# Kernel optimization log

Hardware: AMD Instinct MI355X
Metric: run time of the kernel (lower is better)

The kernel has to match this reference:

```python
import jax, jax.numpy as jnp
import numpy as np

B, L, F, H, VOCAB = 32, 700, 4, 600, 2000  # batch, n_records(max_len), feats/record, hidden, vocab


def setup_inputs() -> dict:
    key = jax.random.key(0)
    ks = jax.random.split(key, 16)
    s = 0.02
    inp = {
        'records': jax.random.randint(ks[0], (B, L, F), 0, VOCAB, dtype=jnp.int64 if jax.config.jax_enable_x64 else jnp.int32),
        'index': jax.random.randint(ks[1], (B,), 0, L, dtype=jnp.int32),
        'emb': jax.random.normal(ks[2], (VOCAB, H), jnp.float32) * s,
        'W_relu': jax.random.normal(ks[3], (4 * H, H), jnp.float32) * s,
        'b_relu': jnp.zeros((H,), jnp.float32),
        'W_lin': jax.random.normal(ks[4], (H, H), jnp.float32) * s,
        'b_lin': jnp.zeros((H,), jnp.float32),
        'W_sig': jax.random.normal(ks[5], (2 * H, H), jnp.float32) * s,
        'b_sig': jnp.zeros((H,), jnp.float32),
        'W_ih': jax.random.normal(ks[6], (H, 4 * H), jnp.float32) * s,
        'W_hh': jax.random.normal(ks[7], (H, 4 * H), jnp.float32) * s,
        'b_ih': jnp.zeros((4 * H,), jnp.float32),
        'b_hh': jnp.zeros((4 * H,), jnp.float32),
        'W_log': jax.random.normal(ks[8], (H, L), jnp.float32) * s,
        'b_log': jnp.zeros((L,), jnp.float32),
    }
    return inp


def _select_content(records, emb, W_relu, b_relu, W_lin, b_lin, W_sig, b_sig):
    # embedding + concat of the 4 record features -> [B, L, 4H]
    embedded = emb[records]                               # [B, L, 4, H]
    emb_cat = embedded.reshape(records.shape[0], records.shape[1], -1)
    emb_relu = jax.nn.relu(emb_cat @ W_relu + b_relu)      # [B, L, H]
    emb_lin = emb_relu @ W_lin + b_lin                     # [B, L, H]
    pre_attn = jnp.einsum('bld,bmd->blm', emb_lin, emb_relu)  # [B, L, L]
    pad = (records.max(axis=2) == 0)                       # [B, L]
    mask = jnp.eye(records.shape[1], dtype=bool)[None] | pad[:, :, None] | pad[:, None, :]
    pre_attn = jnp.where(mask, -jnp.inf, pre_attn)
    attention = jax.nn.softmax(pre_attn, axis=2)
    emb_att = jnp.einsum('blm,bmd->bld', attention, emb_relu)  # [B, L, H]
    gate = jax.nn.sigmoid(jnp.concatenate([emb_relu, emb_att], axis=2) @ W_sig + b_sig)
    return gate * emb_relu                                 # selected_content [B, L, H]


def reference(records, index, emb, W_relu, b_relu, W_lin, b_lin, W_sig, b_sig,
              W_ih, W_hh, b_ih, b_hh, W_log, b_log):
    sc = _select_content(records, emb, W_relu, b_relu, W_lin, b_lin, W_sig, b_sig)
    # init_hidden
    hidden = jnp.mean(sc, axis=1)                          # [B, H]
    cell = jnp.zeros_like(hidden)
    pad_mask = (records.max(axis=2) == 0)                  # [B, L]
    # forward (one pointer step)
    b_idx = jnp.arange(records.shape[0])
    mask = pad_mask.at[b_idx, index].set(True)             # scatter_(1, index, 1)
    x = sc[b_idx, index]                                   # gather -> [B, H]
    gates = x @ W_ih + hidden @ W_hh + b_ih + b_hh         # [B, 4H]
    i, f, g, o = jnp.split(gates, 4, axis=1)               # torch LSTM gate order
    cell = jax.nn.sigmoid(f) * cell + jax.nn.sigmoid(i) * jnp.tanh(g)
    hidden = jax.nn.sigmoid(o) * jnp.tanh(cell)
    logits = hidden @ W_log + b_log                        # [B, max_len]
    masked = jnp.where(mask, -jnp.inf, logits)
    attention = jax.nn.log_softmax(masked, axis=1)         # [B, max_len]
    return attention, hidden, cell
```

## Files before the change

kernel.cpp:

```cpp
#include <hip/hip_runtime.h>
#include <math.h>

typedef unsigned short u16;
typedef _Float16 half8 __attribute__((ext_vector_type(8)));
typedef float f32x4 __attribute__((ext_vector_type(4)));

#define BB 32
#define LL 700
#define HH 600
#define VV 2000
#define H4 2400

#define O_SCAT   0L
#define O_LINH   57344000L
#define O_R1     86016000L
#define O_ATTNH  112896000L
#define O_ERT    144435200L
#define O_EMBH   171468800L
#define O_W2T    174028800L
#define O_WLT    177100800L
#define O_WST    177920000L
#define O_BL     179456000L
#define O_PAD    179458560L
#define O_GATES  179624960L
#define O_WIHT   179932160L
#define O_WLOGT  186076160L
#define O_XCAT   186977280L
#define O_HID16  187059200L
#define O_GLOG   187100160L

__device__ inline u16 f2h(float x) { _Float16 h = (_Float16)x; u16 u; __builtin_memcpy(&u, &h, 2); return u; }
__device__ inline float h2f(u16 u) { _Float16 h; __builtin_memcpy(&h, &u, 2); return (float)h; }
__device__ inline float to_f(float x) { return x; }
__device__ inline float to_f(u16 x) { return h2f(x); }

__device__ __forceinline__ void gll16(const u16* g, u16* l) {
    __builtin_amdgcn_global_load_lds(
        (__attribute__((address_space(1))) void*)g,
        (__attribute__((address_space(3))) void*)l, 16, 0, 0);
}

template<int EPI>
__global__ __launch_bounds__(512, 8) void hgemm_v3(
    const u16* __restrict__ A, const u16* __restrict__ B,
    u16* __restrict__ C16, const float* __restrict__ bias,
    const u16* __restrict__ gate, int ldg,
    int M, int N, int Kp, int lda, int ldb, int ldc,
    long sAz, long sBz, long sCz)
{
    const int bz = blockIdx.z;
    A += sAz * bz;  B += sBz * bz;  C16 += sCz * bz;

    __shared__ __align__(16) u16 As[8192];
    __shared__ __align__(16) u16 Bs[8192];

    const int tid = threadIdx.x;

    const int nx = gridDim.x, ny = gridDim.y;
    const int bid = blockIdx.y * nx + blockIdx.x;
    const int fg  = ny >> 3;
    const int gsz = nx << 3;
    int m_i, n_i;
    if (bid < fg * gsz) {
        int g = bid / gsz, r = bid - g * gsz;
        m_i = (g << 3) + (r & 7);
        n_i = r >> 3;
    } else {
        m_i = bid / nx;
        n_i = bid - m_i * nx;
    }
    const int m0 = m_i << 7, n0 = n_i << 7;

    const int wave = tid >> 6, lane = tid & 63;
    const int fr = lane & 15, q = lane >> 4;
    const int srd = (q ^ ((fr >> 1) & 3)) << 3;
    const int wm = (wave >> 2) << 6;
    const int wn = (wave & 3) << 5;

    const int srow = lane >> 2;
    const int kx   = ((lane & 3) ^ ((srow >> 1) & 3)) << 3;
    int ra = m0 + (wave << 4) + srow;   if (ra > M - 1) ra = M - 1;
    int rb = n0 + (wave << 4) + srow;   if (rb > N - 1) rb = N - 1;
    const u16* gA = A + (long)ra * lda + kx;
    const u16* gB = B + (long)rb * ldb + kx;
    u16* sAw = (u16*)As + (wave << 9);
    u16* sBw = (u16*)Bs + (wave << 9);

    f32x4 acc[4][2];
    #pragma unroll
    for (int i = 0; i < 4; ++i)
        #pragma unroll
        for (int j = 0; j < 2; ++j) acc[i][j] = (f32x4)0.f;

    const int nk = Kp >> 5;

    gll16(gA, sAw);  gll16(gB, sBw);
    __syncthreads();

    for (int t = 0; t < nk; ++t) {
        const int cur = (t & 1) << 12;
        if (t + 1 < nk) {
            const int nxt = cur ^ 4096;
            const long ko = (long)(t + 1) << 5;
            gll16(gA + ko, sAw + nxt);  gll16(gB + ko, sBw + nxt);
        }
        half8 af[4], bf[2];
        #pragma unroll
        for (int i = 0; i < 4; ++i)
            af[i] = *(const half8*)&As[cur + ((wm + (i << 4) + fr) << 5) + srd];
        #pragma unroll
        for (int j = 0; j < 2; ++j)
            bf[j] = *(const half8*)&Bs[cur + ((wn + (j << 4) + fr) << 5) + srd];
        #pragma unroll
        for (int i = 0; i < 4; ++i)
            #pragma unroll
            for (int j = 0; j < 2; ++j)
                acc[i][j] = __builtin_amdgcn_mfma_f32_16x16x32_f16(af[i], bf[j], acc[i][j], 0, 0, 0);
        __syncthreads();
    }

    const int lr = (lane >> 4) << 2;
    #pragma unroll
    for (int j = 0; j < 2; ++j) {
        int n = n0 + wn + (j << 4) + fr;
        if (n >= N) continue;
        float bv = bias ? bias[n] : 0.f;
        #pragma unroll
        for (int i = 0; i < 4; ++i) {
            #pragma unroll
            for (int r = 0; r < 4; ++r) {
                int m = m0 + wm + (i << 4) + lr + r;
                if (m >= M) continue;
                long off = (long)m * ldc + n;
                float v = acc[i][j][r] + bv;
                if (EPI == 1) C16[off] = f2h(v);
                if (EPI == 2) {
                    float sg = 1.f / (1.f + expf(-v));
                    C16[off] = f2h(sg * h2f(gate[(long)m * ldg + n]));
                }
            }
        }
    }
}

__global__ __launch_bounds__(256) void sgemm_k(
    const u16* __restrict__ A, const u16* __restrict__ B, float* __restrict__ C,
    int N, int Kseg, int lda, int ldb, int ldc)
{
    const int wave = threadIdx.x >> 6, lane = threadIdx.x & 63;
    const int fr = lane & 15, q8 = (lane >> 4) << 3;
    int n = blockIdx.x * 64 + wave * 16 + fr;
    int nc = (n < N) ? n : N - 1;
    const int k0 = blockIdx.y * Kseg;
    const u16* pa0 = A + (long)fr * lda + q8;
    const u16* pa1 = A + (long)(fr + 16) * lda + q8;
    const u16* pb  = B + (long)nc * ldb + q8;
    f32x4 acc0 = (f32x4)0.f, acc1 = (f32x4)0.f;
    #pragma unroll 2
    for (int k = k0; k < k0 + Kseg; k += 32) {
        half8 a0 = *(const half8*)(pa0 + k);
        half8 a1 = *(const half8*)(pa1 + k);
        half8 bv = *(const half8*)(pb + k);
        acc0 = __builtin_amdgcn_mfma_f32_16x16x32_f16(a0, bv, acc0, 0, 0, 0);
        acc1 = __builtin_amdgcn_mfma_f32_16x16x32_f16(a1, bv, acc1, 0, 0, 0);
    }
    if (n >= N) return;
    const int mr = (lane >> 4) << 2;
    #pragma unroll
    for (int r = 0; r < 4; ++r) {
        atomicAdd(&C[(long)(mr + r) * ldc + n], acc0[r]);
        atomicAdd(&C[(long)(mr + r + 16) * ldc + n], acc1[r]);
    }
}

__global__ __launch_bounds__(256) void prep_k(
    const float* __restrict__ emb, const float* __restrict__ W_relu,
    const float* __restrict__ W_lin, const float* __restrict__ W_sig,
    const float* __restrict__ W_ih, const float* __restrict__ W_hh,
    const float* __restrict__ W_log, const float* __restrict__ b_lin,
    const float* __restrict__ b_ih, const float* __restrict__ b_hh,
    const float* __restrict__ b_log,
    u16* __restrict__ embh, u16* __restrict__ w2t, u16* __restrict__ wlt,
    u16* __restrict__ wst, u16* __restrict__ wiht, u16* __restrict__ wlogt,
    float* __restrict__ bl640, float* __restrict__ gates, float* __restrict__ glog)
{
    __shared__ float t[32][33];
    const int z = blockIdx.z, bx = blockIdx.x, by = blockIdx.y;
    const int tid = threadIdx.x;

    if (z == 10) {
        int r = by * 32 + (tid >> 5), c = bx * 32 + (tid & 31);
        #pragma unroll
        for (int dy = 0; dy < 32; dy += 8) {
            int rr = r + dy;
            if (rr < VV && c < 640)
                embh[(long)rr * 640 + c] = (c < 600) ? f2h(emb[(long)rr * 600 + c]) : 0;
        }
        return;
    }
    if (z == 11) {
        long idx = ((long)bx * 75 + by) * 256 + tid;
        if (idx < 640) {
            bl640[idx] = (idx < 600) ? b_lin[idx] : 0.f;
        } else if (idx < 640 + (long)BB * H4) {
            long i = idx - 640;
            int n = (int)(i % H4);
            gates[i] = b_ih[n] + b_hh[n];
        } else if (idx < 640 + (long)BB * H4 + (long)BB * 704) {
            long i = idx - 640 - (long)BB * H4;
            int l = (int)(i % 704);
            glog[i] = (l < 700) ? b_log[l] : 0.f;
        }
        return;
    }

    const float* s; u16* d;
    int R, C, lds_, ldo, Rpad, Cpad;
    if (z < 4)      { s = W_relu + 360000L * z; d = w2t + 384000L * z;
                      R = 600; C = 600; lds_ = 600; ldo = 640;  Rpad = 640; Cpad = 600; }
    else if (z == 4){ s = W_lin;           d = wlt;
                      R = 600; C = 600; lds_ = 600; ldo = 640;  Rpad = 640; Cpad = 640; }
    else if (z == 5){ s = W_sig;           d = wst;
                      R = 600; C = 600; lds_ = 600; ldo = 1280; Rpad = 640; Cpad = 600; }
    else if (z == 6){ s = W_sig + 360000;  d = wst + 640;
                      R = 600; C = 600; lds_ = 600; ldo = 1280; Rpad = 640; Cpad = 600; }
    else if (z == 7){ s = W_ih;            d = wiht;
                      R = 600; C = H4;  lds_ = H4;  ldo = 1280; Rpad = 640; Cpad = H4; }
    else if (z == 8){ s = W_hh;            d = wiht + 640;
                      R = 600; C = H4;  lds_ = H4;  ldo = 1280; Rpad = 640; Cpad = H4; }
    else            { s = W_log;           d = wlogt;
                      R = 600; C = 700; lds_ = 700; ldo = 640;  Rpad = 640; Cpad = 704; }

    int r0 = bx * 32, c0 = by * 32;
    if (r0 >= Rpad || c0 >= Cpad) return;
    int tx = tid & 31, ty = tid >> 5;
    #pragma unroll
    for (int dy = 0; dy < 32; dy += 8) {
        int r = r0 + ty + dy, c = c0 + tx;
        t[ty + dy][tx] = (r < R && c < C) ? s[(long)r * lds_ + c] : 0.f;
    }
    __syncthreads();
    #pragma unroll
    for (int dy = 0; dy < 32; dy += 8) {
        int c = c0 + ty + dy, r = r0 + tx;
        if (r < Rpad && c < Cpad) d[(long)c * ldo + r] = f2h(t[tx][ty + dy]);
    }
}

template<typename T>
__global__ __launch_bounds__(256) void transpz_k(
    const T* __restrict__ s, u16* __restrict__ d,
    int R, int C, int lds_, int ldo, int Rpad, int Cpad, long zs_s, long zs_d)
{
    __shared__ float t[32][33];
    s += zs_s * blockIdx.z;  d += zs_d * blockIdx.z;
    int r0 = blockIdx.x * 32, c0 = blockIdx.y * 32;
    int tx = threadIdx.x & 31, ty = threadIdx.x >> 5;
    #pragma unroll
    for (int dy = 0; dy < 32; dy += 8) {
        int r = r0 + ty + dy, c = c0 + tx;
        t[ty + dy][tx] = (r < R && c < C) ? to_f(s[(long)r * lds_ + c]) : 0.f;
    }
    __syncthreads();
    #pragma unroll
    for (int dy = 0; dy < 32; dy += 8) {
        int c = c0 + ty + dy, r = r0 + tx;
        if (r < Rpad && c < Cpad) d[(long)c * ldo + r] = f2h(t[tx][ty + dy]);
    }
}

__global__ __launch_bounds__(320) void gather_relu_k(
    const int* __restrict__ rec, const u16* __restrict__ Ph,
    const float* __restrict__ b_relu, u16* __restrict__ scat, float* __restrict__ pad)
{
    int row = blockIdx.x;
    int t = threadIdx.x;
    int r0 = rec[row * 4 + 0], r1 = rec[row * 4 + 1];
    int r2 = rec[row * 4 + 2], r3 = rec[row * 4 + 3];
    u16* srow = scat + (long)row * 1280;
    if (t < 300) {
        int h = t << 1;
        uint a0 = *(const uint*)&Ph[(long)r0 * H4 + h];
        uint a1 = *(const uint*)&Ph[(long)r1 * H4 + 600 + h];
        uint a2 = *(const uint*)&Ph[(long)r2 * H4 + 1200 + h];
        uint a3 = *(const uint*)&Ph[(long)r3 * H4 + 1800 + h];
        float lo = b_relu[h]     + h2f((u16)a0) + h2f((u16)a1) + h2f((u16)a2) + h2f((u16)a3);
        float hi = b_relu[h + 1] + h2f((u16)(a0 >> 16)) + h2f((u16)(a1 >> 16))
                                 + h2f((u16)(a2 >> 16)) + h2f((u16)(a3 >> 16));
        uint o = (uint)f2h(fmaxf(lo, 0.f)) | ((uint)f2h(fmaxf(hi, 0.f)) << 16);
        *(uint*)&srow[h] = o;
    } else {
        int i = t - 300;
        *(uint*)&srow[600 + (i << 1)]  = 0;
        *(uint*)&srow[1240 + (i << 1)] = 0;
    }
    if (t == 0) {
        int mx = max(max(r0, r1), max(r2, r3));
        pad[row] = (mx == 0) ? 1.f : 0.f;
    }
}

__global__ __launch_bounds__(256) void softmax_w(u16* __restrict__ attnh,
                                                 const float* __restrict__ pad)
{
    const int wave = threadIdx.x >> 6, lane = threadIdx.x & 63;
    const int l = blockIdx.x * 4 + wave, b = blockIdx.y;
    u16* row = attnh + (long)b * (LL * 704) + (long)l * 704;
    const float* pb = pad + b * LL;
    const bool rowpad = pb[l] != 0.f;

    float v[12];
    float mx = -INFINITY;
    #pragma unroll
    for (int i = 0; i < 6; ++i) {
        int e0 = (lane + (i << 6)) << 1;
        float x0 = -INFINITY, x1 = -INFINITY;
        if (e0 < 704) {
            uint u = *(const uint*)&row[e0];
            if (e0 < LL && !(rowpad || e0 == l || pb[e0] != 0.f)) x0 = h2f((u16)u);
            int e1 = e0 + 1;
            if (e1 < LL && !(rowpad || e1 == l || pb[e1] != 0.f)) x1 = h2f((u16)(u >> 16));
        }
        v[2 * i] = x0;  v[2 * i + 1] = x1;
        mx = fmaxf(mx, fmaxf(x0, x1));
    }
    #pragma unroll
    for (int m = 32; m > 0; m >>= 1) mx = fmaxf(mx, __shfl_xor(mx, m));
    mx = fmaxf(mx, -1e30f);

    float sum = 0.f;
    #pragma unroll
    for (int i = 0; i < 12; ++i) { v[i] = expf(v[i] - mx); sum += v[i]; }
    #pragma unroll
    for (int m = 32; m > 0; m >>= 1) sum += __shfl_xor(sum, m);
    float inv = (sum > 0.f) ? 1.f / sum : 0.f;

    #pragma unroll
    for (int i = 0; i < 6; ++i) {
        int e0 = (lane + (i << 6)) << 1;
        if (e0 < 704) {
            uint u = (uint)f2h(v[2 * i] * inv) | ((uint)f2h(v[2 * i + 1] * inv) << 16);
            *(uint*)&row[e0] = u;
        }
    }
}

__global__ __launch_bounds__(256) void xcat_k(const u16* __restrict__ sc,
                                              const int* __restrict__ index,
                                              u16* __restrict__ xcat)
{
    int b = blockIdx.y;
    if (blockIdx.x == 3) {
        const u16* src = sc + ((long)b * LL + index[b]) * HH;
        u16* dst = xcat + b * 1280;
        for (int j = threadIdx.x; j < 1280; j += 256) {
            if (j < 600) dst[j] = src[j];
            else if (j < 640) dst[j] = 0;
            else if (j >= 1240) dst[j] = 0;
        }
        return;
    }
    int h = blockIdx.x * 256 + threadIdx.x;
    if (h >= HH) return;
    float s = 0.f;
    const u16* base = sc + (long)b * LL * HH + h;
    for (int l = 0; l < LL; ++l) s += h2f(base[(long)l * HH]);
    xcat[b * 1280 + 640 + h] = f2h(s * (1.f / 700.f));
}

__global__ void lstm_act_k(const float* __restrict__ gates,
                           float* __restrict__ out_hid, float* __restrict__ out_cell,
                           u16* __restrict__ hid16)
{
    int h = blockIdx.x * 256 + threadIdx.x;
    int b = blockIdx.y;
    if (h >= 640) return;
    if (h >= HH) { hid16[b * 640 + h] = 0; return; }
    const float* g = gates + b * H4;
    float gi = g[h], gg = g[1200 + h], go = g[1800 + h];
    float c = (1.f / (1.f + expf(-gi))) * tanhf(gg);
    float hd = (1.f / (1.f + expf(-go))) * tanhf(c);
    out_hid[b * HH + h] = hd;
    out_cell[b * HH + h] = c;
    hid16[b * 640 + h] = f2h(hd);
}

__global__ __launch_bounds__(256) void logsoftmax_k(const float* __restrict__ glog,
                                                    const float* __restrict__ pad,
                                                    const int* __restrict__ index,
                                                    float* __restrict__ out)
{
    int b = blockIdx.x;
    int t = threadIdx.x;
    int idx = index[b];
    __shared__ float red[256];
    float v[3];
    float mx = -INFINITY;
    #pragma unroll
    for (int ii = 0; ii < 3; ++ii) {
        int l = ii * 256 + t;
        float x = -INFINITY;
        if (l < LL && !(pad[b * LL + l] != 0.f || l == idx)) x = glog[b * 704 + l];
        v[ii] = x;
        mx = fmaxf(mx, x);
    }
    red[t] = mx; __syncthreads();
    for (int s = 128; s > 0; s >>= 1) {
        if (t < s) red[t] = fmaxf(red[t], red[t + s]);
        __syncthreads();
    }
    mx = red[0]; __syncthreads();
    float sum = 0.f;
    #pragma unroll
    for (int ii = 0; ii < 3; ++ii) {
        int l = ii * 256 + t;
        if (l < LL) sum += expf(v[ii] - mx);
    }
    red[t] = sum; __syncthreads();
    for (int s = 128; s > 0; s >>= 1) {
        if (t < s) red[t] += red[t + s];
        __syncthreads();
    }
    float lse = mx + logf(red[0]);
    #pragma unroll
    for (int ii = 0; ii < 3; ++ii) {
        int l = ii * 256 + t;
        if (l < LL) out[b * LL + l] = fmaxf(v[ii] - lse, -1e30f);
    }
}

extern "C" void kernel_launch(void* const* d_in, const int* in_sizes, int n_in,
                              void* d_out, int out_size, void* d_ws, size_t ws_size,
                              hipStream_t stream)
{
    const int*   records = (const int*)d_in[0];
    const int*   index   = (const int*)d_in[1];
    const float* emb     = (const float*)d_in[2];
    const float* W_relu  = (const float*)d_in[3];
    const float* b_relu  = (const float*)d_in[4];
    const float* W_lin   = (const float*)d_in[5];
    const float* b_lin   = (const float*)d_in[6];
    const float* W_sig   = (const float*)d_in[7];
    const float* b_sig   = (const float*)d_in[8];
    const float* W_ih    = (const float*)d_in[9];
    const float* W_hh    = (const float*)d_in[10];
    const float* b_ih    = (const float*)d_in[11];
    const float* b_hh    = (const float*)d_in[12];
    const float* W_log   = (const float*)d_in[13];
    const float* b_log   = (const float*)d_in[14];

    char* ws = (char*)d_ws;
    u16*   scat   = (u16*)(ws + O_SCAT);
    u16*   linh   = (u16*)(ws + O_LINH);
    u16*   Ph     = (u16*)(ws + O_R1);
    u16*   sc16   = (u16*)(ws + O_R1);
    u16*   attnh  = (u16*)(ws + O_ATTNH);
    u16*   erT    = (u16*)(ws + O_ERT);
    u16*   embh   = (u16*)(ws + O_EMBH);
    u16*   w2t    = (u16*)(ws + O_W2T);
    u16*   wlt    = (u16*)(ws + O_WLT);
    u16*   wst    = (u16*)(ws + O_WST);
    float* bl640  = (float*)(ws + O_BL);
    float* pad    = (float*)(ws + O_PAD);
    float* gates  = (float*)(ws + O_GATES);
    u16*   wiht   = (u16*)(ws + O_WIHT);
    u16*   wlogt  = (u16*)(ws + O_WLOGT);
    u16*   xcat   = (u16*)(ws + O_XCAT);
    u16*   hid16  = (u16*)(ws + O_HID16);
    float* glog   = (float*)(ws + O_GLOG);

    float* out      = (float*)d_out;
    float* out_attn = out;
    float* out_hid  = out + BB * LL;
    float* out_cell = out + BB * LL + BB * HH;

    prep_k<<<dim3(20, 75, 12), 256, 0, stream>>>(
        emb, W_relu, W_lin, W_sig, W_ih, W_hh, W_log, b_lin, b_ih, b_hh, b_log,
        embh, w2t, wlt, wst, wiht, wlogt, bl640, gates, glog);

    hgemm_v3<1><<<dim3(19, 16, 1), 512, 0, stream>>>(
        embh, w2t, Ph, nullptr, nullptr, 0,
        VV, H4, 640, 640, 640, H4, 0L, 0L, 0L);

    gather_relu_k<<<dim3(BB * LL), 320, 0, stream>>>(records, Ph, b_relu, scat, pad);

    hgemm_v3<1><<<dim3(5, 175, 1), 512, 0, stream>>>(
        scat, wlt, linh, bl640, nullptr, 0,
        BB * LL, 640, 640, 1280, 640, 640, 0L, 0L, 0L);

    hgemm_v3<1><<<dim3(6, 6, BB), 512, 0, stream>>>(
        linh, scat, attnh, nullptr, nullptr, 0,
        LL, LL, 640, 640, 1280, 704, (long)LL * 640, (long)LL * 1280, (long)LL * 704);

    softmax_w<<<dim3(175, BB), 256, 0, stream>>>(attnh, pad);

    transpz_k<u16><<<dim3(22, 19, BB), 256, 0, stream>>>(
        scat, erT, 700, 600, 1280, 704, 704, 600, (long)700 * 1280, (long)600 * 704);

    hgemm_v3<1><<<dim3(5, 6, BB), 512, 0, stream>>>(
        attnh, erT, scat + 640, nullptr, nullptr, 0,
        LL, HH, 704, 704, 704, 1280, (long)LL * 704, (long)HH * 704, (long)LL * 1280);

    hgemm_v3<2><<<dim3(5, 175, 1), 512, 0, stream>>>(
        scat, wst, sc16, b_sig, scat, 1280,
        BB * LL, HH, 1280, 1280, 1280, 600, 0L, 0L, 0L);

    xcat_k<<<dim3(4, BB), 256, 0, stream>>>(sc16, index, xcat);
    sgemm_k<<<dim3(38, 5), 256, 0, stream>>>(
        xcat, wiht, gates, H4, 256, 1280, 1280, H4);
    lstm_act_k<<<dim3(3, BB), 256, 0, stream>>>(gates, out_hid, out_cell, hid16);
    sgemm_k<<<dim3(11, 5), 256, 0, stream>>>(
        hid16, wlogt, glog, LL, 128, 640, 640, 704);
    logsoftmax_k<<<dim3(BB), 256, 0, stream>>>(glog, pad, index, out_attn);
}
```

Before: 463.4 us.

## Deepen GEMM K-tile to 64 and fuse sequence mean into sigmoid-gate epilogue

The fp16 MFMA GEMM now stages K=64 per iteration instead of 32. That doubles the LDS buffers, uses an 8-way XOR swizzle, issues two async global-to-LDS loads per operand, and drops the occupancy hint from 8 to 4 blocks per CU. It also computes the mean over records of selected_content inside the sigmoid-gate epilogue: per-batch partial sums go through float atomics into a buffer zeroed in prep, replacing xcat_k's strided 700-row reduction. This halves the barrier and loop overhead per K element and removes a full reread of sc. In exchange it costs more LDS, lower occupancy, atomic contention and a non-deterministic summation order. Every call site has Kp divisible by 64 (640, 704, 1280), so the deeper tile needs no padding changes.

```diff
diff --git a/kernel.cpp b/kernel.cpp
--- a/kernel.cpp
+++ b/kernel.cpp
@@ -28,6 +28,7 @@
 #define O_XCAT   186977280L
 #define O_HID16  187059200L
 #define O_GLOG   187100160L
+#define O_XMEAN  187190272L
 
 __device__ inline u16 f2h(float x) { _Float16 h = (_Float16)x; u16 u; __builtin_memcpy(&u, &h, 2); return u; }
 __device__ inline float h2f(u16 u) { _Float16 h; __builtin_memcpy(&h, &u, 2); return (float)h; }
@@ -41,18 +42,19 @@
 }
 
 template<int EPI>
-__global__ __launch_bounds__(512, 8) void hgemm_v3(
+__global__ __launch_bounds__(512, 4) void hgemm_v2(
     const u16* __restrict__ A, const u16* __restrict__ B,
     u16* __restrict__ C16, const float* __restrict__ bias,
     const u16* __restrict__ gate, int ldg,
+    float* __restrict__ xmean,
     int M, int N, int Kp, int lda, int ldb, int ldc,
     long sAz, long sBz, long sCz)
 {
     const int bz = blockIdx.z;
     A += sAz * bz;  B += sBz * bz;  C16 += sCz * bz;
 
-    __shared__ __align__(16) u16 As[8192];
-    __shared__ __align__(16) u16 Bs[8192];
+    __shared__ __align__(16) u16 As[16384];
+    __shared__ __align__(16) u16 Bs[16384];
 
     const int tid = threadIdx.x;
 
@@ -73,18 +75,22 @@
 
     const int wave = tid >> 6, lane = tid & 63;
     const int fr = lane & 15, q = lane >> 4;
-    const int srd = (q ^ ((fr >> 1) & 3)) << 3;
+    const int s0 = (q ^ (fr & 7)) << 3;
     const int wm = (wave >> 2) << 6;
     const int wn = (wave & 3) << 5;
 
-    const int srow = lane >> 2;
-    const int kx   = ((lane & 3) ^ ((srow >> 1) & 3)) << 3;
-    int ra = m0 + (wave << 4) + srow;   if (ra > M - 1) ra = M - 1;
-    int rb = n0 + (wave << 4) + srow;   if (rb > N - 1) rb = N - 1;
-    const u16* gA = A + (long)ra * lda + kx;
-    const u16* gB = B + (long)rb * ldb + kx;
-    u16* sAw = (u16*)As + (wave << 9);
-    u16* sBw = (u16*)Bs + (wave << 9);
+    const int srow = lane >> 3;
+    const int kx   = ((lane & 7) ^ srow) << 3;
+    int ra0 = m0 + (wave << 4) + srow;       if (ra0 > M - 1) ra0 = M - 1;
+    int ra1 = m0 + (wave << 4) + 8 + srow;   if (ra1 > M - 1) ra1 = M - 1;
+    int rb0 = n0 + (wave << 4) + srow;       if (rb0 > N - 1) rb0 = N - 1;
+    int rb1 = n0 + (wave << 4) + 8 + srow;   if (rb1 > N - 1) rb1 = N - 1;
+    const u16* gA0 = A + (long)ra0 * lda + kx;
+    const u16* gA1 = A + (long)ra1 * lda + kx;
+    const u16* gB0 = B + (long)rb0 * ldb + kx;
+    const u16* gB1 = B + (long)rb1 * ldb + kx;
+    u16* sAw = (u16*)As + (wave << 10);
+    u16* sBw = (u16*)Bs + (wave << 10);
 
     f32x4 acc[4][2];
     #pragma unroll
@@ -92,30 +98,36 @@
         #pragma unroll
         for (int j = 0; j < 2; ++j) acc[i][j] = (f32x4)0.f;
 
-    const int nk = Kp >> 5;
-
-    gll16(gA, sAw);  gll16(gB, sBw);
+    const int nk = Kp >> 6;
+
+    gll16(gA0, sAw);  gll16(gA1, sAw + 512);
+    gll16(gB0, sBw);  gll16(gB1, sBw + 512);
     __syncthreads();
 
     for (int t = 0; t < nk; ++t) {
-        const int cur = (t & 1) << 12;
+        const int cur = (t & 1) << 13;
         if (t + 1 < nk) {
-            const int nxt = cur ^ 4096;
-            const long ko = (long)(t + 1) << 5;
-            gll16(gA + ko, sAw + nxt);  gll16(gB + ko, sBw + nxt);
-        }
-        half8 af[4], bf[2];
+            const int nxt = cur ^ 8192;
+            const long ko = (long)(t + 1) << 6;
+            gll16(gA0 + ko, sAw + nxt);  gll16(gA1 + ko, sAw + nxt + 512);
+            gll16(gB0 + ko, sBw + nxt);  gll16(gB1 + ko, sBw + nxt + 512);
+        }
         #pragma unroll
-        for (int i = 0; i < 4; ++i)
-            af[i] = *(const half8*)&As[cur + ((wm + (i << 4) + fr) << 5) + srd];
-        #pragma unroll
-        for (int j = 0; j < 2; ++j)
-            bf[j] = *(const half8*)&Bs[cur + ((wn + (j << 4) + fr) << 5) + srd];
-        #pragma unroll
-        for (int i = 0; i < 4; ++i)
+        for (int half = 0; half < 2; ++half) {
+            const int sh = s0 ^ (half << 5);
+            half8 af[4], bf[2];
+            #pragma unroll
+            for (int i = 0; i < 4; ++i)
+                af[i] = *(const half8*)&As[cur + ((wm + (i << 4) + fr) << 6) + sh];
             #pragma unroll
             for (int j = 0; j < 2; ++j)
-                acc[i][j] = __builtin_amdgcn_mfma_f32_16x16x32_f16(af[i], bf[j], acc[i][j], 0, 0, 0);
+                bf[j] = *(const half8*)&Bs[cur + ((wn + (j << 4) + fr) << 6) + sh];
+            #pragma unroll
+            for (int i = 0; i < 4; ++i)
+                #pragma unroll
+                for (int j = 0; j < 2; ++j)
+                    acc[i][j] = __builtin_amdgcn_mfma_f32_16x16x32_f16(af[i], bf[j], acc[i][j], 0, 0, 0);
+        }
         __syncthreads();
     }
 
@@ -125,6 +137,8 @@
         int n = n0 + wn + (j << 4) + fr;
         if (n >= N) continue;
         float bv = bias ? bias[n] : 0.f;
+        float ps = 0.f;
+        int   cb = -1;
         #pragma unroll
         for (int i = 0; i < 4; ++i) {
             #pragma unroll
@@ -136,10 +150,18 @@
                 if (EPI == 1) C16[off] = f2h(v);
                 if (EPI == 2) {
                     float sg = 1.f / (1.f + expf(-v));
-                    C16[off] = f2h(sg * h2f(gate[(long)m * ldg + n]));
+                    float scv = sg * h2f(gate[(long)m * ldg + n]);
+                    C16[off] = f2h(scv);
+                    int b = m / 700;
+                    if (b != cb) {
+                        if (cb >= 0) atomicAdd(&xmean[cb * 640 + n], ps);
+                        cb = b;  ps = 0.f;
+                    }
+                    ps += scv;
                 }
             }
         }
+        if (EPI == 2 && cb >= 0) atomicAdd(&xmean[cb * 640 + n], ps);
     }
 }
 
@@ -182,7 +204,8 @@
     const float* __restrict__ b_log,
     u16* __restrict__ embh, u16* __restrict__ w2t, u16* __restrict__ wlt,
     u16* __restrict__ wst, u16* __restrict__ wiht, u16* __restrict__ wlogt,
-    float* __restrict__ bl640, float* __restrict__ gates, float* __restrict__ glog)
+    float* __restrict__ bl640, float* __restrict__ gates, float* __restrict__ glog,
+    float* __restrict__ xmean)
 {
     __shared__ float t[32][33];
     const int z = blockIdx.z, bx = blockIdx.x, by = blockIdx.y;
@@ -200,16 +223,21 @@
     }
     if (z == 11) {
         long idx = ((long)bx * 75 + by) * 256 + tid;
+        const long NG = 640 + (long)BB * H4;
+        const long NL = NG + (long)BB * 704;
+        const long NX = NL + (long)BB * 640;
         if (idx < 640) {
             bl640[idx] = (idx < 600) ? b_lin[idx] : 0.f;
-        } else if (idx < 640 + (long)BB * H4) {
+        } else if (idx < NG) {
             long i = idx - 640;
             int n = (int)(i % H4);
             gates[i] = b_ih[n] + b_hh[n];
-        } else if (idx < 640 + (long)BB * H4 + (long)BB * 704) {
-            long i = idx - 640 - (long)BB * H4;
+        } else if (idx < NL) {
+            long i = idx - NG;
             int l = (int)(i % 704);
             glog[i] = (l < 700) ? b_log[l] : 0.f;
+        } else if (idx < NX) {
+            xmean[idx - NL] = 0.f;
         }
         return;
     }
@@ -347,6 +375,7 @@
 
 __global__ __launch_bounds__(256) void xcat_k(const u16* __restrict__ sc,
                                               const int* __restrict__ index,
+                                              const float* __restrict__ xmean,
                                               u16* __restrict__ xcat)
 {
     int b = blockIdx.y;
@@ -362,10 +391,7 @@
     }
     int h = blockIdx.x * 256 + threadIdx.x;
     if (h >= HH) return;
-    float s = 0.f;
-    const u16* base = sc + (long)b * LL * HH + h;
-    for (int l = 0; l < LL; ++l) s += h2f(base[(long)l * HH]);
-    xcat[b * 1280 + 640 + h] = f2h(s * (1.f / 700.f));
+    xcat[b * 1280 + 640 + h] = f2h(xmean[b * 640 + h] * (1.f / 700.f));
 }
 
 __global__ void lstm_act_k(const float* __restrict__ gates,
@@ -468,6 +494,7 @@
     u16*   xcat   = (u16*)(ws + O_XCAT);
     u16*   hid16  = (u16*)(ws + O_HID16);
     float* glog   = (float*)(ws + O_GLOG);
+    float* xmean  = (float*)(ws + O_XMEAN);
 
     float* out      = (float*)d_out;
     float* out_attn = out;
@@ -476,20 +503,20 @@
 
     prep_k<<<dim3(20, 75, 12), 256, 0, stream>>>(
         emb, W_relu, W_lin, W_sig, W_ih, W_hh, W_log, b_lin, b_ih, b_hh, b_log,
-        embh, w2t, wlt, wst, wiht, wlogt, bl640, gates, glog);
-
-    hgemm_v3<1><<<dim3(19, 16, 1), 512, 0, stream>>>(
-        embh, w2t, Ph, nullptr, nullptr, 0,
+        embh, w2t, wlt, wst, wiht, wlogt, bl640, gates, glog, xmean);
+
+    hgemm_v2<1><<<dim3(19, 16, 1), 512, 0, stream>>>(
+        embh, w2t, Ph, nullptr, nullptr, 0, nullptr,
         VV, H4, 640, 640, 640, H4, 0L, 0L, 0L);
 
     gather_relu_k<<<dim3(BB * LL), 320, 0, stream>>>(records, Ph, b_relu, scat, pad);
 
-    hgemm_v3<1><<<dim3(5, 175, 1), 512, 0, stream>>>(
-        scat, wlt, linh, bl640, nullptr, 0,
+    hgemm_v2<1><<<dim3(5, 175, 1), 512, 0, stream>>>(
+        scat, wlt, linh, bl640, nullptr, 0, nullptr,
         BB * LL, 640, 640, 1280, 640, 640, 0L, 0L, 0L);
 
-    hgemm_v3<1><<<dim3(6, 6, BB), 512, 0, stream>>>(
-        linh, scat, attnh, nullptr, nullptr, 0,
+    hgemm_v2<1><<<dim3(6, 6, BB), 512, 0, stream>>>(
+        linh, scat, attnh, nullptr, nullptr, 0, nullptr,
         LL, LL, 640, 640, 1280, 704, (long)LL * 640, (long)LL * 1280, (long)LL * 704);
 
     softmax_w<<<dim3(175, BB), 256, 0, stream>>>(attnh, pad);
@@ -497,15 +524,15 @@
     transpz_k<u16><<<dim3(22, 19, BB), 256, 0, stream>>>(
         scat, erT, 700, 600, 1280, 704, 704, 600, (long)700 * 1280, (long)600 * 704);
 
-    hgemm_v3<1><<<dim3(5, 6, BB), 512, 0, stream>>>(
-        attnh, erT, scat + 640, nullptr, nullptr, 0,
+    hgemm_v2<1><<<dim3(5, 6, BB), 512, 0, stream>>>(
+        attnh, erT, scat + 640, nullptr, nullptr, 0, nullptr,
         LL, HH, 704, 704, 704, 1280, (long)LL * 704, (long)HH * 704, (long)LL * 1280);
 
-    hgemm_v3<2><<<dim3(5, 175, 1), 512, 0, stream>>>(
-        scat, wst, sc16, b_sig, scat, 1280,
+    hgemm_v2<2><<<dim3(5, 175, 1), 512, 0, stream>>>(
+        scat, wst, sc16, b_sig, scat, 1280, xmean,
         BB * LL, HH, 1280, 1280, 1280, 600, 0L, 0L, 0L);
 
-    xcat_k<<<dim3(4, BB), 256, 0, stream>>>(sc16, index, xcat);
+    xcat_k<<<dim3(4, BB), 256, 0, stream>>>(sc16, index, xmean, xcat);
     sgemm_k<<<dim3(38, 5), 256, 0, stream>>>(
         xcat, wiht, gates, H4, 256, 1280, 1280, H4);
     lstm_act_k<<<dim3(3, BB), 256, 0, stream>>>(gates, out_hid, out_cell, hid16);
```

Result: faster. 426.9 us (-7.9%).
